# Kernel tuning notes

Hardware: AMD Instinct MI355X
Metric: run time of the kernel (lower is better)

The kernel has to match this reference:

```python
import jax, jax.numpy as jnp
import numpy as np

S = 17          # grid size = 544/32
A = 5           # num anchors
C = 20          # num classes
B = 256         # batch
G = 32          # GT boxes per image (distinct cells, sorted)
HW = S * S
IOU_THRESH = 0.6
OBJ_SCALE, NOOBJ_SCALE, COORD_SCALE, CLS_SCALE = 5.0, 1.0, 1.0, 1.0
ANCHORS = np.array([[1.3221, 1.73145], [3.19275, 4.00944], [5.05587, 8.09892],
                    [9.47112, 4.84053], [11.2364, 10.0071]], dtype=np.float32)


def setup_inputs() -> dict:
    key = jax.random.key(0)
    k1, k2, k3 = jax.random.split(key, 3)
    bbox_pred = jax.random.uniform(k1, (B, HW, A, 4), dtype=jnp.float32)
    iou_pred = jax.random.uniform(k2, (B, HW, A, 1), dtype=jnp.float32)
    score_pred = jax.random.uniform(k3, (B, HW, A, C), dtype=jnp.float32)
    # Structured targets: per image, G GT boxes in G distinct cells, sorted by
    # linear cell index (matches the implicit assumption of the torch code
    # that pairs sorted true-cells with GT-ordered anchor indices).
    rng = np.random.default_rng(0)
    tg = np.zeros((B, G, 6), np.float32)
    for b in range(B):
        cells = np.sort(rng.permutation(HW)[:G])
        ci, cj = cells // S, cells % S
        u = rng.uniform(0.2, 0.8, (G, 2))
        cx = (ci + u[:, 0]) / S
        cy = (cj + u[:, 1]) / S
        w = rng.uniform(0.05, 0.25, G).astype(np.float32)
        h = rng.uniform(0.05, 0.25, G).astype(np.float32)
        tg[b, :, 0] = b
        tg[b, :, 1] = rng.integers(0, C, G)
        tg[b, :, 2] = cx - w / 2
        tg[b, :, 3] = cy - h / 2
        tg[b, :, 4] = cx + w / 2
        tg[b, :, 5] = cy + h / 2
    return {"bbox_pred": bbox_pred, "iou_pred": iou_pred, "score_pred": score_pred,
            "targets": jnp.asarray(tg.reshape(B * G, 6)),
            "anchors": jnp.asarray(ANCHORS)}


def _box_iou(a, b):
    # a: [N,4], b: [G,4] corner boxes -> [N,G]
    lt = jnp.maximum(a[:, None, :2], b[None, :, :2])
    rb = jnp.minimum(a[:, None, 2:], b[None, :, 2:])
    wh = jnp.clip(rb - lt, 0.0)
    inter = wh[..., 0] * wh[..., 1]
    area_a = (a[:, 2] - a[:, 0]) * (a[:, 3] - a[:, 1])
    area_b = (b[:, 2] - b[:, 0]) * (b[:, 3] - b[:, 1])
    return inter / (area_a[:, None] + area_b[None, :] - inter)


def _forward(bbox_pred, iou_pred, score_pred, targets, anchors):
    anc = anchors / 17.0
    # decode predicted boxes: xy offset + cell index, wh scaled by anchors
    gi, gj = jnp.meshgrid(jnp.arange(S), jnp.arange(S), indexing="ij")
    c_map = jnp.stack([gi, gj], axis=-1).astype(bbox_pred.dtype)[None, :, :, None, :]
    p5 = bbox_pred.reshape(B, S, S, A, 4)
    xy = (p5[..., :2] + c_map) / S
    wh = p5[..., 2:] * anc[None, None, None] / S
    c_box = jnp.concatenate([xy, wh], axis=-1).reshape(B, HW * A, 4)
    pred_b = jnp.concatenate([c_box[..., :2] - c_box[..., 2:] / 2,
                              c_box[..., :2] + c_box[..., 2:] / 2], axis=-1)
    tgt = targets.reshape(B, G, 6)

    def per_image(bbox_p, iou_p, score_p, pb, t):
        gt_class = t[:, 1].astype(jnp.int32)
        gt_box = t[:, 2:]                               # corner, normalized
        gt_cxy = (gt_box[:, :2] + gt_box[:, 2:]) / 2    # b_box_to_c_box
        gt_wh = gt_box[:, 2:] - gt_box[:, :2]
        c_xy = gt_cxy * S
        c_ij = jnp.floor(c_xy).astype(jnp.int32)
        offset_xy = c_xy - c_ij
        tar_gt_box = jnp.concatenate([offset_xy, gt_wh], axis=-1)
        # distinct+sorted cells by construction -> dedup keeps all G boxes
        cells = c_ij[:, 0] * S + c_ij[:, 1]             # [G]
        iou = _box_iou(pb, gt_box)                      # [HW*A, G]
        best_iou = iou.max(axis=1).reshape(HW, A, 1)
        iou_mask = jnp.where(best_iou <= IOU_THRESH, NOOBJ_SCALE * (0.0 - iou_p), 0.0)
        # anchor wh vs gt wh IoU -> best anchor per GT
        inter = (jnp.minimum(anc[:, None, 0], gt_wh[None, :, 0]) *
                 jnp.minimum(anc[:, None, 1], gt_wh[None, :, 1]))
        a_area = anc[:, 0] * anc[:, 1]
        g_area = gt_wh[:, 0] * gt_wh[:, 1]
        anchor_iou = inter / (a_area[:, None] + g_area[None, :] - inter)
        anchor_index = anchor_iou.argmax(axis=0)        # [G]
        iou3 = iou.reshape(HW, A, G)
        gidx = jnp.arange(G)
        iou_mask = iou_mask.at[cells, anchor_index, 0].set(
            OBJ_SCALE * (1.0 - iou_p[cells, anchor_index, 0]))
        iou_t = jnp.zeros((HW, A, 1), bbox_p.dtype).at[cells, anchor_index, 0].set(
            iou3[cells, anchor_index, gidx])
        box_mask = jnp.full((HW, A, 1), 0.01, bbox_p.dtype).at[cells, anchor_index, 0].set(COORD_SCALE)
        boxes_t = jnp.concatenate([jnp.full((HW, A, 2), 0.5, bbox_p.dtype),
                                   jnp.ones((HW, A, 2), bbox_p.dtype)], axis=-1)
        boxes_t = boxes_t.at[cells, anchor_index].set(tar_gt_box)
        class_mask = jnp.zeros((HW, A, 1), bbox_p.dtype).at[cells, anchor_index, 0].set(CLS_SCALE)
        class_t = jnp.zeros((HW, A, C), bbox_p.dtype).at[cells, anchor_index, gt_class].set(1.0)
        box_l = jnp.sum((bbox_p * box_mask - boxes_t * box_mask) ** 2) / G
        iou_l = jnp.sum((iou_p * iou_mask - iou_t * iou_mask) ** 2) / G
        cls_l = jnp.sum((score_p * class_mask - class_t * class_mask) ** 2) / G
        return box_l + iou_l + cls_l

    return jnp.sum(jax.vmap(per_image)(bbox_pred, iou_pred, score_pred, pred_b, tgt))


def reference(bbox_pred, iou_pred, score_pred, targets, anchors):
    return _forward(bbox_pred, iou_pred, score_pred, targets, anchors)
```

## Files before the change

kernel.cpp:

```cpp
#include <hip/hip_runtime.h>

#define SS 17
#define AA 5
#define CC 20
#define BATCH 256
#define GG 32
#define HWC (SS * SS)
#define NP (HWC * AA)
#define SPLIT 4
#define NTHREADS 256
#define NPART (BATCH * SPLIT)

__global__ __launch_bounds__(NTHREADS) void yolo_loss_kernel(
    const float* __restrict__ bbox,
    const float* __restrict__ ioup,
    const float* __restrict__ score,
    const float* __restrict__ tgt,
    const float* __restrict__ anchors,
    float* __restrict__ part)
{
    const int b   = blockIdx.x;
    const int spl = blockIdx.y;
    const int tid = threadIdx.x;

    __shared__ float gx1[GG], gy1[GG], gx2[GG], gy2[GG], garea[GG];
    __shared__ float tarb[GG][4];
    __shared__ int   gcls[GG];
    __shared__ float anc[AA][2];
    __shared__ short assign[NP + 1];
    __shared__ float wsum[NTHREADS / 64];

    for (int p = tid; p < NP; p += NTHREADS) assign[p] = -1;
    if (tid < AA * 2) ((float*)anc)[tid] = anchors[tid] * (1.0f / 17.0f);
    __syncthreads();

    if (tid < GG) {
        const float* t = tgt + (size_t)(b * GG + tid) * 6;
        int   cls = (int)t[1];
        float x1 = t[2], y1 = t[3], x2 = t[4], y2 = t[5];
        float cx = (x1 + x2) * 0.5f, cy = (y1 + y2) * 0.5f;
        float gw = x2 - x1, gh = y2 - y1;
        float cxs = cx * (float)SS, cys = cy * (float)SS;
        int ci = (int)floorf(cxs), cj = (int)floorf(cys);
        gx1[tid] = x1; gy1[tid] = y1; gx2[tid] = x2; gy2[tid] = y2;
        garea[tid] = gw * gh;
        tarb[tid][0] = cxs - (float)ci;
        tarb[tid][1] = cys - (float)cj;
        tarb[tid][2] = gw;
        tarb[tid][3] = gh;
        gcls[tid] = cls;
        float best = -1.0f; int bi = 0;
        for (int a = 0; a < AA; a++) {
            float aw = anc[a][0], ah = anc[a][1];
            float inter = fminf(aw, gw) * fminf(ah, gh);
            float u = aw * ah + gw * gh - inter;
            float v = inter / u;
            if (v > best) { best = v; bi = a; }
        }
        int cell = ci * SS + cj;
        assign[cell * AA + bi] = (short)tid;
    }
    __syncthreads();

    float acc = 0.0f;
    const int base = b * NP;
    for (int p = spl * NTHREADS + tid; p < NP; p += NTHREADS * SPLIT) {
        float4 bb = ((const float4*)bbox)[base + p];
        float  ip = ioup[base + p];
        int hw = p / AA;
        int a  = p - hw * AA;
        int i  = hw / SS;
        int j  = hw - i * SS;

        float px = (bb.x + (float)i) * (1.0f / SS);
        float py = (bb.y + (float)j) * (1.0f / SS);
        float pw = bb.z * anc[a][0] * (1.0f / SS);
        float ph = bb.w * anc[a][1] * (1.0f / SS);
        float px1 = px - pw * 0.5f, py1 = py - ph * 0.5f;
        float px2 = px + pw * 0.5f, py2 = py + ph * 0.5f;
        float parea = (px2 - px1) * (py2 - py1);

        int ga = (int)assign[p];
        float best = 0.0f;
        float iou_t = 0.0f;
        #pragma unroll 8
        for (int g = 0; g < GG; g++) {
            float lx = fmaxf(px1, gx1[g]);
            float ly = fmaxf(py1, gy1[g]);
            float rx = fminf(px2, gx2[g]);
            float ry = fminf(py2, gy2[g]);
            float w  = fmaxf(rx - lx, 0.0f);
            float h  = fmaxf(ry - ly, 0.0f);
            float inter = w * h;
            float iou = inter / (parea + garea[g] - inter);
            best = fmaxf(best, iou);
            if (g == ga) iou_t = iou;
        }

        if (ga >= 0) {
            float dx = bb.x - tarb[ga][0];
            float dy = bb.y - tarb[ga][1];
            float dw = bb.z - tarb[ga][2];
            float dh = bb.w - tarb[ga][3];
            acc += dx * dx + dy * dy + dw * dw + dh * dh;
            float m = 5.0f * (1.0f - ip);
            float d = ip - iou_t;
            acc += (m * m) * (d * d);
            const float4* sp4 = (const float4*)(score + (size_t)(base + p) * CC);
            int cls = gcls[ga];
            float csum = 0.0f;
            #pragma unroll
            for (int c4 = 0; c4 < CC / 4; c4++) {
                float4 sv = sp4[c4];
                float v0 = sv.x - (4 * c4 + 0 == cls ? 1.0f : 0.0f);
                float v1 = sv.y - (4 * c4 + 1 == cls ? 1.0f : 0.0f);
                float v2 = sv.z - (4 * c4 + 2 == cls ? 1.0f : 0.0f);
                float v3 = sv.w - (4 * c4 + 3 == cls ? 1.0f : 0.0f);
                csum += v0 * v0 + v1 * v1 + v2 * v2 + v3 * v3;
            }
            acc += csum;
        } else {
            float dx = bb.x - 0.5f, dy = bb.y - 0.5f;
            float dw = bb.z - 1.0f, dh = bb.w - 1.0f;
            acc += 1e-4f * (dx * dx + dy * dy + dw * dw + dh * dh);
            if (best <= 0.6f) {
                float q = ip * ip;
                acc += q * q;
            }
        }
    }

    #pragma unroll
    for (int off = 32; off > 0; off >>= 1)
        acc += __shfl_down(acc, off, 64);
    if ((tid & 63) == 0) wsum[tid >> 6] = acc;
    __syncthreads();
    if (tid == 0) {
        float s = 0.0f;
        #pragma unroll
        for (int w = 0; w < NTHREADS / 64; w++) s += wsum[w];
        part[b * SPLIT + spl] = s;
    }
}

__global__ __launch_bounds__(NTHREADS) void yolo_reduce_kernel(
    const float* __restrict__ part, float* __restrict__ out)
{
    const int tid = threadIdx.x;
    __shared__ float wsum[NTHREADS / 64];
    float s = 0.0f;
    #pragma unroll
    for (int k = 0; k < NPART / NTHREADS; k++)
        s += part[k * NTHREADS + tid];
    #pragma unroll
    for (int off = 32; off > 0; off >>= 1)
        s += __shfl_down(s, off, 64);
    if ((tid & 63) == 0) wsum[tid >> 6] = s;
    __syncthreads();
    if (tid == 0) {
        float t = 0.0f;
        #pragma unroll
        for (int w = 0; w < NTHREADS / 64; w++) t += wsum[w];
        out[0] = t * (1.0f / (float)GG);
    }
}

extern "C" void kernel_launch(void* const* d_in, const int* in_sizes, int n_in,
                              void* d_out, int out_size, void* d_ws, size_t ws_size,
                              hipStream_t stream) {
    const float* bbox    = (const float*)d_in[0];
    const float* ioup    = (const float*)d_in[1];
    const float* score   = (const float*)d_in[2];
    const float* tgt     = (const float*)d_in[3];
    const float* anchors = (const float*)d_in[4];
    float* out  = (float*)d_out;
    float* part = (float*)d_ws;

    dim3 grid(BATCH, SPLIT);
    yolo_loss_kernel<<<grid, NTHREADS, 0, stream>>>(bbox, ioup, score, tgt, anchors, part);
    yolo_reduce_kernel<<<1, NTHREADS, 0, stream>>>(part, out);
}
```

Baseline: 91.94 us.

## Replace per-GT IoU divisions with division-free threshold test and chunked two-point threads

The ignore-mask test best_iou<=0.6 is rewritten as a sign check of inter-0.375*(parea+garea), removing 32 divisions per prediction; the exact IoU is computed only for the assigned GT. Each block now takes a contiguous chunk of predictions, with each thread handling two points whose loads are issued before the GT loop, and GT boxes are packed as float4 in shared memory. The algebraic rewrite assumes positive union areas and may differ at exact threshold ties.

Result: faster. 88.65 us (-3.6%).

```diff
diff --git a/kernel.cpp b/kernel.cpp
--- a/kernel.cpp
+++ b/kernel.cpp
@@ -8,6 +8,7 @@
 #define HWC (SS * SS)
 #define NP (HWC * AA)
 #define SPLIT 4
+#define CHUNK 362
 #define NTHREADS 256
 #define NPART (BATCH * SPLIT)
 
@@ -23,12 +24,12 @@
     const int spl = blockIdx.y;
     const int tid = threadIdx.x;
 
-    __shared__ float gx1[GG], gy1[GG], gx2[GG], gy2[GG], garea[GG];
-    __shared__ float tarb[GG][4];
-    __shared__ int   gcls[GG];
-    __shared__ float anc[AA][2];
-    __shared__ short assign[NP + 1];
-    __shared__ float wsum[NTHREADS / 64];
+    __shared__ float4 gbox[GG];
+    __shared__ float4 tarb[GG];
+    __shared__ int    gcls[GG];
+    __shared__ float  anc[AA][2];
+    __shared__ short  assign[NP + 3];
+    __shared__ float  wsum[NTHREADS / 64];
 
     for (int p = tid; p < NP; p += NTHREADS) assign[p] = -1;
     if (tid < AA * 2) ((float*)anc)[tid] = anchors[tid] * (1.0f / 17.0f);
@@ -42,91 +43,147 @@
         float gw = x2 - x1, gh = y2 - y1;
         float cxs = cx * (float)SS, cys = cy * (float)SS;
         int ci = (int)floorf(cxs), cj = (int)floorf(cys);
-        gx1[tid] = x1; gy1[tid] = y1; gx2[tid] = x2; gy2[tid] = y2;
-        garea[tid] = gw * gh;
-        tarb[tid][0] = cxs - (float)ci;
-        tarb[tid][1] = cys - (float)cj;
-        tarb[tid][2] = gw;
-        tarb[tid][3] = gh;
+        gbox[tid] = make_float4(x1, y1, x2, y2);
+        tarb[tid] = make_float4(cxs - (float)ci, cys - (float)cj, gw, gh);
         gcls[tid] = cls;
         float best = -1.0f; int bi = 0;
         for (int a = 0; a < AA; a++) {
             float aw = anc[a][0], ah = anc[a][1];
             float inter = fminf(aw, gw) * fminf(ah, gh);
-            float u = aw * ah + gw * gh - inter;
-            float v = inter / u;
+            float v = inter / (aw * ah + gw * gh - inter);
             if (v > best) { best = v; bi = a; }
         }
-        int cell = ci * SS + cj;
-        assign[cell * AA + bi] = (short)tid;
-    }
-    __syncthreads();
+        assign[(ci * SS + cj) * AA + bi] = (short)tid;
+    }
+    __syncthreads();
+
+    const int pbase = spl * CHUNK;
+    const int pend  = min(NP, pbase + CHUNK);
+    const int gbase = b * NP;
+
+    const int p0 = pbase + tid;
+    const int p1 = p0 + NTHREADS;
+    const bool v1 = (p1 < pend);
+    const int p1c = v1 ? p1 : p0;
+
+    float4 bb0 = ((const float4*)bbox)[gbase + p0];
+    float4 bb1 = ((const float4*)bbox)[gbase + p1c];
+    float  ip0 = ioup[gbase + p0];
+    float  ip1 = ioup[gbase + p1c];
+
+    float px10, py10, px20, py20, pa0;
+    float px11, py11, px21, py21, pa1;
+    {
+        int hw = p0 / AA, a = p0 - hw * AA;
+        int i = hw / SS,  j = hw - i * SS;
+        float px = (bb0.x + (float)i) * (1.0f / SS);
+        float py = (bb0.y + (float)j) * (1.0f / SS);
+        float pw = bb0.z * anc[a][0] * (1.0f / SS);
+        float ph = bb0.w * anc[a][1] * (1.0f / SS);
+        px10 = px - pw * 0.5f; py10 = py - ph * 0.5f;
+        px20 = px + pw * 0.5f; py20 = py + ph * 0.5f;
+        pa0  = (px20 - px10) * (py20 - py10);
+    }
+    {
+        int hw = p1c / AA, a = p1c - hw * AA;
+        int i = hw / SS,   j = hw - i * SS;
+        float px = (bb1.x + (float)i) * (1.0f / SS);
+        float py = (bb1.y + (float)j) * (1.0f / SS);
+        float pw = bb1.z * anc[a][0] * (1.0f / SS);
+        float ph = bb1.w * anc[a][1] * (1.0f / SS);
+        px11 = px - pw * 0.5f; py11 = py - ph * 0.5f;
+        px21 = px + pw * 0.5f; py21 = py + ph * 0.5f;
+        pa1  = (px21 - px11) * (py21 - py11);
+    }
+
+    float any0 = -1.0f, any1 = -1.0f;
+    #pragma unroll 8
+    for (int g = 0; g < GG; g++) {
+        float4 gb = gbox[g];
+        float garea = (gb.z - gb.x) * (gb.w - gb.y);
+        {
+            float w = fminf(px20, gb.z) - fmaxf(px10, gb.x);
+            float h = fminf(py20, gb.w) - fmaxf(py10, gb.y);
+            float inter = fmaxf(w, 0.0f) * fmaxf(h, 0.0f);
+            any0 = fmaxf(any0, __builtin_fmaf(-0.375f, pa0 + garea, inter));
+        }
+        {
+            float w = fminf(px21, gb.z) - fmaxf(px11, gb.x);
+            float h = fminf(py21, gb.w) - fmaxf(py11, gb.y);
+            float inter = fmaxf(w, 0.0f) * fmaxf(h, 0.0f);
+            any1 = fmaxf(any1, __builtin_fmaf(-0.375f, pa1 + garea, inter));
+        }
+    }
 
     float acc = 0.0f;
-    const int base = b * NP;
-    for (int p = spl * NTHREADS + tid; p < NP; p += NTHREADS * SPLIT) {
-        float4 bb = ((const float4*)bbox)[base + p];
-        float  ip = ioup[base + p];
-        int hw = p / AA;
-        int a  = p - hw * AA;
-        int i  = hw / SS;
-        int j  = hw - i * SS;
-
-        float px = (bb.x + (float)i) * (1.0f / SS);
-        float py = (bb.y + (float)j) * (1.0f / SS);
-        float pw = bb.z * anc[a][0] * (1.0f / SS);
-        float ph = bb.w * anc[a][1] * (1.0f / SS);
-        float px1 = px - pw * 0.5f, py1 = py - ph * 0.5f;
-        float px2 = px + pw * 0.5f, py2 = py + ph * 0.5f;
-        float parea = (px2 - px1) * (py2 - py1);
-
-        int ga = (int)assign[p];
-        float best = 0.0f;
-        float iou_t = 0.0f;
-        #pragma unroll 8
-        for (int g = 0; g < GG; g++) {
-            float lx = fmaxf(px1, gx1[g]);
-            float ly = fmaxf(py1, gy1[g]);
-            float rx = fminf(px2, gx2[g]);
-            float ry = fminf(py2, gy2[g]);
-            float w  = fmaxf(rx - lx, 0.0f);
-            float h  = fmaxf(ry - ly, 0.0f);
+
+    {
+        int ga = (int)assign[p0];
+        if (ga >= 0) {
+            float4 gb = gbox[ga];
+            float w = fmaxf(fminf(px20, gb.z) - fmaxf(px10, gb.x), 0.0f);
+            float h = fmaxf(fminf(py20, gb.w) - fmaxf(py10, gb.y), 0.0f);
             float inter = w * h;
-            float iou = inter / (parea + garea[g] - inter);
-            best = fmaxf(best, iou);
-            if (g == ga) iou_t = iou;
-        }
-
-        if (ga >= 0) {
-            float dx = bb.x - tarb[ga][0];
-            float dy = bb.y - tarb[ga][1];
-            float dw = bb.z - tarb[ga][2];
-            float dh = bb.w - tarb[ga][3];
+            float garea = (gb.z - gb.x) * (gb.w - gb.y);
+            float iou_t = inter / (pa0 + garea - inter);
+            float4 tb = tarb[ga];
+            float dx = bb0.x - tb.x, dy = bb0.y - tb.y;
+            float dw = bb0.z - tb.z, dh = bb0.w - tb.w;
             acc += dx * dx + dy * dy + dw * dw + dh * dh;
-            float m = 5.0f * (1.0f - ip);
-            float d = ip - iou_t;
+            float m = 5.0f * (1.0f - ip0);
+            float d = ip0 - iou_t;
             acc += (m * m) * (d * d);
-            const float4* sp4 = (const float4*)(score + (size_t)(base + p) * CC);
+            const float4* sp4 = (const float4*)(score + (size_t)(gbase + p0) * CC);
             int cls = gcls[ga];
-            float csum = 0.0f;
             #pragma unroll
             for (int c4 = 0; c4 < CC / 4; c4++) {
                 float4 sv = sp4[c4];
                 float v0 = sv.x - (4 * c4 + 0 == cls ? 1.0f : 0.0f);
-                float v1 = sv.y - (4 * c4 + 1 == cls ? 1.0f : 0.0f);
+                float v1v = sv.y - (4 * c4 + 1 == cls ? 1.0f : 0.0f);
                 float v2 = sv.z - (4 * c4 + 2 == cls ? 1.0f : 0.0f);
                 float v3 = sv.w - (4 * c4 + 3 == cls ? 1.0f : 0.0f);
-                csum += v0 * v0 + v1 * v1 + v2 * v2 + v3 * v3;
+                acc += v0 * v0 + v1v * v1v + v2 * v2 + v3 * v3;
             }
-            acc += csum;
         } else {
-            float dx = bb.x - 0.5f, dy = bb.y - 0.5f;
-            float dw = bb.z - 1.0f, dh = bb.w - 1.0f;
+            float dx = bb0.x - 0.5f, dy = bb0.y - 0.5f;
+            float dw = bb0.z - 1.0f, dh = bb0.w - 1.0f;
             acc += 1e-4f * (dx * dx + dy * dy + dw * dw + dh * dh);
-            if (best <= 0.6f) {
-                float q = ip * ip;
-                acc += q * q;
+            if (any0 <= 0.0f) { float q = ip0 * ip0; acc += q * q; }
+        }
+    }
+
+    if (v1) {
+        int ga = (int)assign[p1];
+        if (ga >= 0) {
+            float4 gb = gbox[ga];
+            float w = fmaxf(fminf(px21, gb.z) - fmaxf(px11, gb.x), 0.0f);
+            float h = fmaxf(fminf(py21, gb.w) - fmaxf(py11, gb.y), 0.0f);
+            float inter = w * h;
+            float garea = (gb.z - gb.x) * (gb.w - gb.y);
+            float iou_t = inter / (pa1 + garea - inter);
+            float4 tb = tarb[ga];
+            float dx = bb1.x - tb.x, dy = bb1.y - tb.y;
+            float dw = bb1.z - tb.z, dh = bb1.w - tb.w;
+            acc += dx * dx + dy * dy + dw * dw + dh * dh;
+            float m = 5.0f * (1.0f - ip1);
+            float d = ip1 - iou_t;
+            acc += (m * m) * (d * d);
+            const float4* sp4 = (const float4*)(score + (size_t)(gbase + p1) * CC);
+            int cls = gcls[ga];
+            #pragma unroll
+            for (int c4 = 0; c4 < CC / 4; c4++) {
+                float4 sv = sp4[c4];
+                float v0 = sv.x - (4 * c4 + 0 == cls ? 1.0f : 0.0f);
+                float v1v = sv.y - (4 * c4 + 1 == cls ? 1.0f : 0.0f);
+                float v2 = sv.z - (4 * c4 + 2 == cls ? 1.0f : 0.0f);
+                float v3 = sv.w - (4 * c4 + 3 == cls ? 1.0f : 0.0f);
+                acc += v0 * v0 + v1v * v1v + v2 * v2 + v3 * v3;
             }
+        } else {
+            float dx = bb1.x - 0.5f, dy = bb1.y - 0.5f;
+            float dw = bb1.z - 1.0f, dh = bb1.w - 1.0f;
+            acc += 1e-4f * (dx * dx + dy * dy + dw * dw + dh * dh);
+            if (any1 <= 0.0f) { float q = ip1 * ip1; acc += q * q; }
         }
     }
 
@@ -135,12 +192,8 @@
         acc += __shfl_down(acc, off, 64);
     if ((tid & 63) == 0) wsum[tid >> 6] = acc;
     __syncthreads();
-    if (tid == 0) {
-        float s = 0.0f;
-        #pragma unroll
-        for (int w = 0; w < NTHREADS / 64; w++) s += wsum[w];
-        part[b * SPLIT + spl] = s;
-    }
+    if (tid == 0)
+        part[b * SPLIT + spl] = wsum[0] + wsum[1] + wsum[2] + wsum[3];
 }
 
 __global__ __launch_bounds__(NTHREADS) void yolo_reduce_kernel(
@@ -157,12 +210,8 @@
         s += __shfl_down(s, off, 64);
     if ((tid & 63) == 0) wsum[tid >> 6] = s;
     __syncthreads();
-    if (tid == 0) {
-        float t = 0.0f;
-        #pragma unroll
-        for (int w = 0; w < NTHREADS / 64; w++) t += wsum[w];
-        out[0] = t * (1.0f / (float)GG);
-    }
+    if (tid == 0)
+        out[0] = (wsum[0] + wsum[1] + wsum[2] + wsum[3]) * (1.0f / (float)GG);
 }
 
 extern "C" void kernel_launch(void* const* d_in, const int* in_sizes, int n_in,
@@ -177,6 +226,7 @@
     float* part = (float*)d_ws;
 
     dim3 grid(BATCH, SPLIT);
-    yolo_loss_kernel<<<grid, NTHREADS, 0, stream>>>(bbox, ioup, score, tgt, anchors, part);
+    yolo_loss_kernel<<<grid, NTHREADS, 0, stream>>>(bbox, ioup, score, tgt,
+                                                    anchors, part);
     yolo_reduce_kernel<<<1, NTHREADS, 0, stream>>>(part, out);
 }
```
